# Kernel optimization log

Hardware: AMD Instinct MI355X
Metric: run time of the kernel (lower is better)

The kernel has to match this reference:

```python
import jax, jax.numpy as jnp
import numpy as np

IN_DIM = 512
HEADS = 8
HEAD_DIM = IN_DIM // HEADS
SCALE = HEAD_DIM ** -0.5


def setup_inputs() -> dict:
    key = jax.random.key(0)
    ks = jax.random.split(key, 9)
    B, C, H, W = 16, IN_DIM, 32, 32
    std = 1.0 / np.sqrt(C)  # ~ conv2d default init scale
    inp = {
        "x": jax.random.normal(ks[0], (B, C, H, W), dtype=jnp.float32),
        "wq": jax.random.normal(ks[1], (C, C), dtype=jnp.float32) * std,
        "bq": jax.random.normal(ks[2], (C,), dtype=jnp.float32) * std,
        "wk": jax.random.normal(ks[3], (C, C), dtype=jnp.float32) * std,
        "bk": jax.random.normal(ks[4], (C,), dtype=jnp.float32) * std,
        "wv": jax.random.normal(ks[5], (C, C), dtype=jnp.float32) * std,
        "bv": jax.random.normal(ks[6], (C,), dtype=jnp.float32) * std,
        "wo": jax.random.normal(ks[7], (C, C), dtype=jnp.float32) * std,
        "bo": jax.random.normal(ks[8], (C,), dtype=jnp.float32) * std,
        "gamma": jnp.zeros((1,), dtype=jnp.float32) + 0.1,  # learned residual scale
    }
    return inp


def reference(x, wq, bq, wk, bk, wv, bv, wo, bo, gamma):
    B, C, H, W = x.shape
    N = H * W
    hd = HEAD_DIM
    # flatten spatial: [B, C, N]
    xf = x.reshape(B, C, N)
    # 1x1 convs == channel matmuls: [B, C, N]
    q = jnp.einsum('oc,bcn->bon', wq, xf) + bq[None, :, None]
    k = jnp.einsum('oc,bcn->bon', wk, xf) + bk[None, :, None]
    v = jnp.einsum('oc,bcn->bon', wv, xf) + bv[None, :, None]
    # split heads: [B, heads, head_dim, N]
    q = q.reshape(B, HEADS, hd, N)
    k = k.reshape(B, HEADS, hd, N)
    v = v.reshape(B, HEADS, hd, N)
    # energy[b,h,i,j] = sum_d q[b,h,d,i] * k[b,h,d,j]
    energy = jnp.einsum('bhdi,bhdj->bhij', q, k) * SCALE
    attn = jax.nn.softmax(energy, axis=-1)  # [B, heads, N, N]
    # out[b,h,d,i] = sum_j attn[b,h,i,j] * v[b,h,d,j]
    out = jnp.einsum('bhij,bhdj->bhdi', attn, v)
    out = out.reshape(B, C, N)
    out = jnp.einsum('oc,bcn->bon', wo, out) + bo[None, :, None]
    y = gamma[0] * out.reshape(B, C, H, W) + x
    return y
```

## Files before the change

### kernel.cpp

```cpp
#include <hip/hip_runtime.h>
#include <hip/hip_bf16.h>

#define BB 16
#define CC 512
#define HH 8
#define DD 64
#define NN 1024

using f32x4  = __attribute__((ext_vector_type(4))) float;
typedef __bf16 bf16x8 __attribute__((ext_vector_type(8)));
typedef __bf16 bf16x4 __attribute__((ext_vector_type(4)));

#define MFMA16(a, b, c) __builtin_amdgcn_mfma_f32_16x16x32_bf16((a), (b), (c), 0, 0, 0)

#define WAITVM16 asm volatile("s_waitcnt vmcnt(16)" ::: "memory")
#define WAITVM8  asm volatile("s_waitcnt vmcnt(8)" ::: "memory")
#define WAITVM4  asm volatile("s_waitcnt vmcnt(4)" ::: "memory")
#define WAITVM0  asm volatile("s_waitcnt vmcnt(0)" ::: "memory")
#define BARRIER __builtin_amdgcn_s_barrier()
#define SCHEDB  __builtin_amdgcn_sched_barrier(0)

__device__ __forceinline__ void glds16(const __hip_bfloat16* g, __hip_bfloat16* l) {
  typedef __attribute__((address_space(1))) const void gv_t;
  typedef __attribute__((address_space(3))) void lv_t;
  __builtin_amdgcn_global_load_lds((gv_t*)g, (lv_t*)l, 16, 0, 0);
}

__global__ __launch_bounds__(256) void k_prep(
    const float* __restrict__ x, __hip_bfloat16* __restrict__ xT,
    __hip_bfloat16* __restrict__ xbf,
    const float* __restrict__ wq, const float* __restrict__ wk,
    const float* __restrict__ wv, const float* __restrict__ wo,
    __hip_bfloat16* __restrict__ wqb) {
  __shared__ float tile[64][65];
  const int L = blockIdx.x;
  const int t = threadIdx.x;
  if (L >= 2048) {
    const int j = L - 2048;
    const int mat = j >> 8;
    const float* s = (mat == 0) ? wq : (mat == 1) ? wk : (mat == 2) ? wv : wo;
    __hip_bfloat16* o = wqb + (size_t)mat * CC * CC;
    const int i = ((j & 255) * 256 + t) * 4;
    float4 v = *(const float4*)(s + i);
    alignas(8) __hip_bfloat16 tm[4];
    tm[0] = __float2bfloat16(v.x);
    tm[1] = __float2bfloat16(v.y);
    tm[2] = __float2bfloat16(v.z);
    tm[3] = __float2bfloat16(v.w);
    *(bf16x4*)(o + i) = *(const bf16x4*)tm;
    return;
  }
  const int c = L & 7, r = L >> 3;
  const int b  = c * 2 + (r >> 7);
  const int rr = r & 127;
  const int bn = (rr & 15) * 64;
  const int bc = (rr >> 4) * 64;

  const float* xb = x + ((size_t)b * CC + bc) * NN + bn;
  __hip_bfloat16* xbo = xbf + ((size_t)b * CC + bc) * NN + bn;
  const int r0 = t >> 4;
  const int c0 = (t & 15) * 4;
  for (int p = 0; p < 4; ++p) {
    const int rw = r0 + p * 16;
    float4 v = *(const float4*)(xb + (size_t)rw * NN + c0);
    tile[rw][c0 + 0] = v.x;
    tile[rw][c0 + 1] = v.y;
    tile[rw][c0 + 2] = v.z;
    tile[rw][c0 + 3] = v.w;
    alignas(8) __hip_bfloat16 tm[4];
    tm[0] = __float2bfloat16(v.x);
    tm[1] = __float2bfloat16(v.y);
    tm[2] = __float2bfloat16(v.z);
    tm[3] = __float2bfloat16(v.w);
    *(bf16x4*)(xbo + (size_t)rw * NN + c0) = *(const bf16x4*)tm;
  }
  __syncthreads();

  __hip_bfloat16* xo = xT + ((size_t)b * NN + bn) * CC + bc;
  const int rn0 = t >> 3;
  const int cc0 = (t & 7) * 8;
  for (int p = 0; p < 2; ++p) {
    const int rn = rn0 + p * 32;
    alignas(16) __hip_bfloat16 tmp[8];
    for (int j = 0; j < 8; ++j) tmp[j] = __float2bfloat16(tile[cc0 + j][rn]);
    *(bf16x8*)(xo + (size_t)rn * CC + cc0) = *(const bf16x8*)tmp;
  }
}

__global__ __launch_bounds__(256, 2) void k_gemm_qkv(
    const __hip_bfloat16* __restrict__ Wqkv,
    const __hip_bfloat16* __restrict__ Xt,
    const float* __restrict__ bq, const float* __restrict__ bk,
    const float* __restrict__ bv,
    __hip_bfloat16* __restrict__ qT, __hip_bfloat16* __restrict__ kT,
    __hip_bfloat16* __restrict__ vO, float qscale) {
  __shared__ __hip_bfloat16 Wl[2][8192];
  __shared__ __hip_bfloat16 Xl[2][8192];
  const int bid = blockIdx.x;
  const int by0 = bid >> 7;
  const int bx  = bid & 127;
  const int nt  = bx * 128;
  const int bb  = nt >> 10;
  const int nb  = nt & 1023;
  const int t  = threadIdx.x;
  const int w  = t >> 6, l = t & 63;
  const int wr = w >> 1, wc = w & 1;
  const int lg = l >> 4, lr16 = l & 15;

  f32x4 acc[4][4] = {};

  const int srow = w * 8 + (l >> 3);
  const int scol = ((l & 7) ^ ((l >> 3) & 7)) * 8;
  const __hip_bfloat16* wsrc0 = Wqkv + (size_t)(by0 * 128 + srow) * CC + scol;
  const __hip_bfloat16* xsrc  = Xt + ((size_t)nt + srow) * CC + scol;

  auto STAGE = [&](int bn, int ktg) {
    const int rep = ktg >> 3;
    const int k0  = (ktg & 7) * 64;
    const __hip_bfloat16* ws = wsrc0 + (size_t)rep * 512 * CC;
#pragma unroll
    for (int i = 0; i < 4; ++i)
      glds16(ws + (size_t)(i * 32) * CC + k0, &Wl[bn][(w * 8 + i * 32) * 64]);
#pragma unroll
    for (int i = 0; i < 4; ++i)
      glds16(xsrc + (size_t)(i * 32) * CC + k0, &Xl[bn][(w * 8 + i * 32) * 64]);
  };

  const int s7 = lr16 & 7;
  const int slot0 = ((lg) ^ s7) * 8;
  const int slot1 = ((4 + lg) ^ s7) * 8;
  const int rowA = (wr * 64 + lr16) * 64;
  const int rowB = (wc * 64 + lr16) * 64;

  auto STEP = [&](int bn) {
    const __hip_bfloat16* Wb = &Wl[bn][0];
    const __hip_bfloat16* Xb = &Xl[bn][0];
#pragma unroll
    for (int ks = 0; ks < 2; ++ks) {
      const int sl = ks ? slot1 : slot0;
      bf16x8 af[4], bfr[4];
#pragma unroll
      for (int mi = 0; mi < 4; ++mi) af[mi] = *(const bf16x8*)(Wb + rowA + mi * 1024 + sl);
#pragma unroll
      for (int nj = 0; nj < 4; ++nj) bfr[nj] = *(const bf16x8*)(Xb + rowB + nj * 1024 + sl);
      __builtin_amdgcn_s_setprio(1);
#pragma unroll
      for (int mi = 0; mi < 4; ++mi)
#pragma unroll
        for (int nj = 0; nj < 4; ++nj)
          acc[mi][nj] = MFMA16(af[mi], bfr[nj], acc[mi][nj]);
      __builtin_amdgcn_s_setprio(0);
    }
  };

  STAGE(0, 0);
  STAGE(1, 1);
  for (int ktg = 0; ktg < 24; ++ktg) {
    if (ktg == 23)                    { WAITVM0;  }
    else if (ktg > 0 && (ktg & 7) == 0) { WAITVM16; }
    else                              { WAITVM8;  }
    BARRIER; SCHEDB;
    STEP(ktg & 1);
    BARRIER;
    if (ktg < 22) STAGE(ktg & 1, ktg + 2);

    if ((ktg & 7) == 7) {
      const int rep = ktg >> 3;
      const float* bias = (rep == 0) ? bq : (rep == 1) ? bk : bv;
      const float scale = (rep == 0) ? qscale : 1.0f;
      __hip_bfloat16* outT = (rep == 0) ? qT : kT;
#pragma unroll
      for (int mi = 0; mi < 4; ++mi) {
        const int o0 = by0 * 128 + wr * 64 + mi * 16 + lg * 4;
#pragma unroll
        for (int nj = 0; nj < 4; ++nj) {
          const int n = nb + wc * 64 + nj * 16 + lr16;
          if (rep < 2) {
            alignas(8) __hip_bfloat16 tmp[4];
#pragma unroll
            for (int rj = 0; rj < 4; ++rj)
              tmp[rj] = __float2bfloat16((acc[mi][nj][rj] + bias[o0 + rj]) * scale);
            const int hh = o0 >> 6, d0 = o0 & 63;
            *(bf16x4*)(outT + (((size_t)(bb * HH + hh)) * NN + n) * DD + d0) =
                *(const bf16x4*)tmp;
          } else {
#pragma unroll
            for (int rj = 0; rj < 4; ++rj)
              vO[((size_t)bb * CC + o0 + rj) * NN + n] =
                  __float2bfloat16(acc[mi][nj][rj] + bias[o0 + rj]);
          }
        }
      }
      if (ktg < 23) {
#pragma unroll
        for (int mi = 0; mi < 4; ++mi)
#pragma unroll
          for (int nj = 0; nj < 4; ++nj)
            acc[mi][nj] = f32x4{0.f, 0.f, 0.f, 0.f};
      }
    }
  }
}

__global__ __launch_bounds__(256, 4) void k_gemm_o(
    const __hip_bfloat16* __restrict__ W,
    const __hip_bfloat16* __restrict__ Xt,
    const float* __restrict__ bias,
    const __hip_bfloat16* __restrict__ xbf,
    const float* __restrict__ gamma,
    float* __restrict__ y) {
  __shared__ __hip_bfloat16 Wl[2][4096];
  __shared__ __hip_bfloat16 Xl[2][4096];
  const int b  = blockIdx.z;
  const int ot = blockIdx.y * 128;
  const int nt = blockIdx.x * 128;
  const int t  = threadIdx.x;
  const int w  = t >> 6, l = t & 63;
  const int wr = w >> 1, wc = w & 1;
  const int lg = l >> 4, lr16 = l & 15;

  f32x4 acc[4][4] = {};

  const int srow = w * 16 + (l >> 2);
  const int scol = ((l & 3) ^ ((l >> 3) & 3)) * 8;
  const __hip_bfloat16* ws0 = W + (size_t)(ot + srow) * CC + scol;
  const __hip_bfloat16* xs0 = Xt + ((size_t)b * NN + nt + srow) * CC + scol;

  const int sx  = (lg ^ ((lr16 >> 1) & 3)) * 8;
  const int rdA = (wr * 64 + lr16) * 32 + sx;
  const int rdB = (wc * 64 + lr16) * 32 + sx;

#define STAGEO(bn, k0)                                        \
  do {                                                        \
    glds16(ws0 + (k0), &Wl[bn][w * 512]);                     \
    glds16(ws0 + (size_t)64 * CC + (k0), &Wl[bn][2048 + w * 512]); \
    glds16(xs0 + (k0), &Xl[bn][w * 512]);                     \
    glds16(xs0 + (size_t)64 * CC + (k0), &Xl[bn][2048 + w * 512]); \
  } while (0)

  STAGEO(0, 0);
  for (int kt = 0; kt < 16; ++kt) {
    WAITVM0;
    BARRIER; SCHEDB;
    if (kt < 15) STAGEO((kt + 1) & 1, (kt + 1) * 32);
    const __hip_bfloat16* Wb = &Wl[kt & 1][0];
    const __hip_bfloat16* Xb = &Xl[kt & 1][0];
    bf16x8 af[4], bfr[4];
#pragma unroll
    for (int mi = 0; mi < 4; ++mi) af[mi] = *(const bf16x8*)(Wb + rdA + mi * 512);
#pragma unroll
    for (int nj = 0; nj < 4; ++nj) bfr[nj] = *(const bf16x8*)(Xb + rdB + nj * 512);
    __builtin_amdgcn_s_setprio(1);
#pragma unroll
    for (int mi = 0; mi < 4; ++mi)
#pragma unroll
      for (int nj = 0; nj < 4; ++nj)
        acc[mi][nj] = MFMA16(af[mi], bfr[nj], acc[mi][nj]);
    __builtin_amdgcn_s_setprio(0);
  }
#undef STAGEO

  const float g = gamma[0];
  for (int mi = 0; mi < 4; ++mi) {
    const int o0 = ot + wr * 64 + mi * 16 + lg * 4;
    for (int nj = 0; nj < 4; ++nj) {
      const int n = nt + wc * 64 + nj * 16 + lr16;
      for (int rj = 0; rj < 4; ++rj) {
        const size_t idx = ((size_t)b * CC + o0 + rj) * NN + n;
        y[idx] = g * (acc[mi][nj][rj] + bias[o0 + rj]) + __bfloat162float(xbf[idx]);
      }
    }
  }
}

__global__ __launch_bounds__(256, 2) void k_attn(
    const __hip_bfloat16* __restrict__ qT,
    const __hip_bfloat16* __restrict__ kT,
    const __hip_bfloat16* __restrict__ v,
    __hip_bfloat16* __restrict__ attT) {
  __shared__ __hip_bfloat16 Kl[3][4096];
  __shared__ __hip_bfloat16 Vl[3][4096];

  const int L = blockIdx.x;
  const int c = L & 7, s = L >> 3;
  const int bh = c * 16 + (s >> 2);
  const int i0 = (s & 3) * 256;
  const int b = bh >> 3, h = bh & 7;
  const int t  = threadIdx.x;
  const int w  = t >> 6, l = t & 63;
  const int lg = l >> 4, lr = l & 15;

  const __hip_bfloat16* qb = qT + ((size_t)(b * HH + h)) * NN * DD;
  const __hip_bfloat16* kb = kT + ((size_t)(b * HH + h)) * NN * DD;
  const __hip_bfloat16* vb = v + ((size_t)b * CC + h * DD) * NN;

  bf16x8 qf[4][2];
#pragma unroll
  for (int g = 0; g < 4; ++g) {
    const __hip_bfloat16* qp = qb + (size_t)(i0 + w * 64 + g * 16 + lr) * DD + lg * 8;
    qf[g][0] = *(const bf16x8*)qp;
    qf[g][1] = *(const bf16x8*)(qp + 32);
  }

  const int rA = w * 8 + (l >> 3);
  const int rB = rA + 32;
  const int sA = (l & 7) ^ ((rA & 3) ^ (((rA >> 3) & 1) << 2));
  const __hip_bfloat16* gKA = kb + rA * DD + sA * 8;
  const __hip_bfloat16* gKB = kb + rB * DD + sA * 8;
  const __hip_bfloat16* gVA = vb + (size_t)rA * NN + sA * 8;
  const __hip_bfloat16* gVB = vb + (size_t)rB * NN + sA * 8;

  auto STAGE = [&](int bufn, int tile) {
    glds16(gKA + (size_t)tile * 4096, &Kl[bufn][w * 512]);
    glds16(gKB + (size_t)tile * 4096, &Kl[bufn][2048 + w * 512]);
    glds16(gVA + tile * 64, &Vl[bufn][w * 512]);
    glds16(gVB + tile * 64, &Vl[bufn][2048 + w * 512]);
  };

  const int swzK = (lr & 3) ^ (((lr >> 2) & 1) << 2);
  const int krl  = 8 * (lr >> 2) + (lr & 3);
  const int offK0 = krl * 64 + ((lg ^ swzK) * 8);
  const int offK1 = krl * 64 + (((lg + 4) ^ swzK) * 8);
  const int swzV = (lr & 3) ^ (((lr >> 3) & 1) << 2);

  f32x4 accO[4][4] = {};
  f32x4 accL[4] = {};
  f32x4 st[4][4];
  bf16x8 pf[4][2];
  const bf16x8 ones = {(__bf16)1.f, (__bf16)1.f, (__bf16)1.f, (__bf16)1.f,
                       (__bf16)1.f, (__bf16)1.f, (__bf16)1.f, (__bf16)1.f};

  auto QK = [&](const __hip_bfloat16* Kb) {
    __builtin_amdgcn_s_setprio(1);
#pragma unroll
    for (int jt = 0; jt < 4; ++jt) {
      const int jo = (jt >> 1) * 2048 + (jt & 1) * 256;
      bf16x8 kf0 = *(const bf16x8*)(Kb + jo + offK0);
      bf16x8 kf1 = *(const bf16x8*)(Kb + jo + offK1);
#pragma unroll
      for (int g = 0; g < 4; ++g) {
        f32x4 a = {};
        a = MFMA16(kf0, qf[g][0], a);
        a = MFMA16(kf1, qf[g][1], a);
        st[g][jt] = a;
      }
    }
    __builtin_amdgcn_s_setprio(0);
  };

  auto EXP = [&]() {
#pragma unroll
    for (int g = 0; g < 4; ++g) {
      union { bf16x8 v8; __hip_bfloat16 h[8]; } pk0, pk1;
#pragma unroll
      for (int jt = 0; jt < 4; ++jt)
#pragma unroll
        for (int rj = 0; rj < 4; ++rj) {
          const float p = __builtin_amdgcn_exp2f(st[g][jt][rj]);
          if (jt < 2) pk0.h[(jt & 1) * 4 + rj] = __float2bfloat16(p);
          else        pk1.h[(jt & 1) * 4 + rj] = __float2bfloat16(p);
        }
      pf[g][0] = pk0.v8;
      pf[g][1] = pk1.v8;
    }
  };

  auto PV = [&](const __hip_bfloat16* Vb) {
    __builtin_amdgcn_s_setprio(1);
#pragma unroll
    for (int ks = 0; ks < 2; ++ks) {
#pragma unroll
      for (int dt = 0; dt < 4; ++dt) {
        bf16x8 vf = *(const bf16x8*)(Vb + (dt * 16 + lr) * 64 + (((ks * 4 + lg) ^ swzV) * 8));
#pragma unroll
        for (int g = 0; g < 4; ++g)
          accO[g][dt] = MFMA16(pf[g][ks], vf, accO[g][dt]);
      }
#pragma unroll
      for (int g = 0; g < 4; ++g)
        accL[g] = MFMA16(pf[g][ks], ones, accL[g]);
    }
    __builtin_amdgcn_s_setprio(0);
  };

  STAGE(0, 0);
  STAGE(1, 1);
  STAGE(2, 2);
  WAITVM8;
  BARRIER;
  QK(&Kl[0][0]);
  EXP();

  for (int tl = 0; tl < 16; ++tl) {
    const int cur = tl % 3;
    if (tl < 15) {
      if (tl < 14) { WAITVM4; } else { WAITVM0; }
      BARRIER; SCHEDB;
      QK(&Kl[(tl + 1) % 3][0]);
      PV(&Vl[cur][0]);
      EXP();
      BARRIER;
      if (tl < 13) STAGE(cur, tl + 3);
    } else {
      PV(&Vl[cur][0]);
    }
  }

#pragma unroll
  for (int g = 0; g < 4; ++g)
#pragma unroll
    for (int dt = 0; dt < 4; ++dt) {
      f32x4 o;
#pragma unroll
      for (int rj = 0; rj < 4; ++rj) o[rj] = accO[g][dt][rj] / accL[g][rj];
#pragma unroll
      for (int rj = 0; rj < 4; ++rj) {
        const int i = i0 + w * 64 + g * 16 + 4 * lg + rj;
        const int d = dt * 16 + lr;
        attT[((size_t)b * NN + i) * CC + h * DD + d] = __float2bfloat16(o[rj]);
      }
    }
}

extern "C" void kernel_launch(void* const* d_in, const int* in_sizes, int n_in,
                              void* d_out, int out_size, void* d_ws, size_t ws_size,
                              hipStream_t stream) {
  const float* x     = (const float*)d_in[0];
  const float* wq    = (const float*)d_in[1];
  const float* bq    = (const float*)d_in[2];
  const float* wk    = (const float*)d_in[3];
  const float* bk    = (const float*)d_in[4];
  const float* wv    = (const float*)d_in[5];
  const float* bv    = (const float*)d_in[6];
  const float* wo    = (const float*)d_in[7];
  const float* bo    = (const float*)d_in[8];
  const float* gamma = (const float*)d_in[9];
  float* y = (float*)d_out;

  char* ws = (char*)d_ws;
  const size_t szT = (size_t)BB * NN * CC * 2;
  __hip_bfloat16* xT  = (__hip_bfloat16*)(ws);
  __hip_bfloat16* qT  = (__hip_bfloat16*)(ws + szT);
  __hip_bfloat16* kTb = (__hip_bfloat16*)(ws + 2 * szT);
  __hip_bfloat16* vB  = (__hip_bfloat16*)(ws + 3 * szT);
  __hip_bfloat16* xbf = (__hip_bfloat16*)(ws + 4 * szT);
  __hip_bfloat16* wqb = (__hip_bfloat16*)(ws + 5 * szT);
  __hip_bfloat16* wob = wqb + (size_t)3 * CC * CC;

  k_prep<<<dim3(2048 + 1024), 256, 0, stream>>>(x, xT, xbf, wq, wk, wv, wo, wqb);

  const float qsc = 0.125f * 1.44269504f;
  k_gemm_qkv<<<dim3(512), 256, 0, stream>>>(
      wqb, xT, bq, bk, bv, qT, kTb, vB, qsc);

  k_attn<<<dim3(BB * HH * (NN / 256)), 256, 0, stream>>>(qT, kTb, vB, xT);

  k_gemm_o<<<dim3(NN / 128, CC / 128, BB), 256, 0, stream>>>(
      wob, xT, bo, xbf, gamma, y);
}
```

Measured before the change: 109.7 us.

## Split QKV GEMM into one block per output tile, single-buffered

The QKV projection kernel previously had each of 512 blocks loop over Q, K and V weight sectors using a double-buffered LDS pipeline. Now 1536 blocks each compute one 128x128 output tile over K=512 with a single LDS buffer and a full vmcnt(0) wait every k-step. Occupancy is raised to 4 blocks per CU. This gives more parallelism and less LDS per block, but drops the load/compute overlap within a block and reloads the X tile three times.

New measurement: 111.3 us. Within noise of the previous version (+1.5%).

```diff
diff --git a/kernel.cpp b/kernel.cpp
--- a/kernel.cpp
+++ b/kernel.cpp
@@ -13,7 +13,6 @@
 
 #define MFMA16(a, b, c) __builtin_amdgcn_mfma_f32_16x16x32_bf16((a), (b), (c), 0, 0, 0)
 
-#define WAITVM16 asm volatile("s_waitcnt vmcnt(16)" ::: "memory")
 #define WAITVM8  asm volatile("s_waitcnt vmcnt(8)" ::: "memory")
 #define WAITVM4  asm volatile("s_waitcnt vmcnt(4)" ::: "memory")
 #define WAITVM0  asm volatile("s_waitcnt vmcnt(0)" ::: "memory")
@@ -87,18 +86,19 @@
   }
 }
 
-__global__ __launch_bounds__(256, 2) void k_gemm_qkv(
+__global__ __launch_bounds__(256, 4) void k_gemm_qkv(
     const __hip_bfloat16* __restrict__ Wqkv,
     const __hip_bfloat16* __restrict__ Xt,
     const float* __restrict__ bq, const float* __restrict__ bk,
     const float* __restrict__ bv,
     __hip_bfloat16* __restrict__ qT, __hip_bfloat16* __restrict__ kT,
     __hip_bfloat16* __restrict__ vO, float qscale) {
-  __shared__ __hip_bfloat16 Wl[2][8192];
-  __shared__ __hip_bfloat16 Xl[2][8192];
+  __shared__ __hip_bfloat16 Wl[8192];
+  __shared__ __hip_bfloat16 Xl[8192];
   const int bid = blockIdx.x;
-  const int by0 = bid >> 7;
+  const int by  = bid >> 7;
   const int bx  = bid & 127;
+  const int sector = by >> 2;
   const int nt  = bx * 128;
   const int bb  = nt >> 10;
   const int nb  = nt & 1023;
@@ -111,20 +111,8 @@
 
   const int srow = w * 8 + (l >> 3);
   const int scol = ((l & 7) ^ ((l >> 3) & 7)) * 8;
-  const __hip_bfloat16* wsrc0 = Wqkv + (size_t)(by0 * 128 + srow) * CC + scol;
-  const __hip_bfloat16* xsrc  = Xt + ((size_t)nt + srow) * CC + scol;
-
-  auto STAGE = [&](int bn, int ktg) {
-    const int rep = ktg >> 3;
-    const int k0  = (ktg & 7) * 64;
-    const __hip_bfloat16* ws = wsrc0 + (size_t)rep * 512 * CC;
-#pragma unroll
-    for (int i = 0; i < 4; ++i)
-      glds16(ws + (size_t)(i * 32) * CC + k0, &Wl[bn][(w * 8 + i * 32) * 64]);
-#pragma unroll
-    for (int i = 0; i < 4; ++i)
-      glds16(xsrc + (size_t)(i * 32) * CC + k0, &Xl[bn][(w * 8 + i * 32) * 64]);
-  };
+  const __hip_bfloat16* wsrc = Wqkv + (size_t)(by * 128 + srow) * CC + scol;
+  const __hip_bfloat16* xsrc = Xt + ((size_t)nt + srow) * CC + scol;
 
   const int s7 = lr16 & 7;
   const int slot0 = ((lg) ^ s7) * 8;
@@ -132,17 +120,24 @@
   const int rowA = (wr * 64 + lr16) * 64;
   const int rowB = (wc * 64 + lr16) * 64;
 
-  auto STEP = [&](int bn) {
-    const __hip_bfloat16* Wb = &Wl[bn][0];
-    const __hip_bfloat16* Xb = &Xl[bn][0];
+  for (int kt = 0; kt < 8; ++kt) {
+    const int k0 = kt * 64;
+#pragma unroll
+    for (int i = 0; i < 4; ++i)
+      glds16(wsrc + (size_t)(i * 32) * CC + k0, &Wl[(w * 8 + i * 32) * 64]);
+#pragma unroll
+    for (int i = 0; i < 4; ++i)
+      glds16(xsrc + (size_t)(i * 32) * CC + k0, &Xl[(w * 8 + i * 32) * 64]);
+    WAITVM0;
+    BARRIER; SCHEDB;
 #pragma unroll
     for (int ks = 0; ks < 2; ++ks) {
       const int sl = ks ? slot1 : slot0;
       bf16x8 af[4], bfr[4];
 #pragma unroll
-      for (int mi = 0; mi < 4; ++mi) af[mi] = *(const bf16x8*)(Wb + rowA + mi * 1024 + sl);
-#pragma unroll
-      for (int nj = 0; nj < 4; ++nj) bfr[nj] = *(const bf16x8*)(Xb + rowB + nj * 1024 + sl);
+      for (int mi = 0; mi < 4; ++mi) af[mi] = *(const bf16x8*)(Wl + rowA + mi * 1024 + sl);
+#pragma unroll
+      for (int nj = 0; nj < 4; ++nj) bfr[nj] = *(const bf16x8*)(Xl + rowB + nj * 1024 + sl);
       __builtin_amdgcn_s_setprio(1);
 #pragma unroll
       for (int mi = 0; mi < 4; ++mi)
@@ -151,52 +146,33 @@
           acc[mi][nj] = MFMA16(af[mi], bfr[nj], acc[mi][nj]);
       __builtin_amdgcn_s_setprio(0);
     }
-  };
-
-  STAGE(0, 0);
-  STAGE(1, 1);
-  for (int ktg = 0; ktg < 24; ++ktg) {
-    if (ktg == 23)                    { WAITVM0;  }
-    else if (ktg > 0 && (ktg & 7) == 0) { WAITVM16; }
-    else                              { WAITVM8;  }
-    BARRIER; SCHEDB;
-    STEP(ktg & 1);
     BARRIER;
-    if (ktg < 22) STAGE(ktg & 1, ktg + 2);
-
-    if ((ktg & 7) == 7) {
-      const int rep = ktg >> 3;
-      const float* bias = (rep == 0) ? bq : (rep == 1) ? bk : bv;
-      const float scale = (rep == 0) ? qscale : 1.0f;
-      __hip_bfloat16* outT = (rep == 0) ? qT : kT;
-#pragma unroll
-      for (int mi = 0; mi < 4; ++mi) {
-        const int o0 = by0 * 128 + wr * 64 + mi * 16 + lg * 4;
-#pragma unroll
-        for (int nj = 0; nj < 4; ++nj) {
-          const int n = nb + wc * 64 + nj * 16 + lr16;
-          if (rep < 2) {
-            alignas(8) __hip_bfloat16 tmp[4];
-#pragma unroll
-            for (int rj = 0; rj < 4; ++rj)
-              tmp[rj] = __float2bfloat16((acc[mi][nj][rj] + bias[o0 + rj]) * scale);
-            const int hh = o0 >> 6, d0 = o0 & 63;
-            *(bf16x4*)(outT + (((size_t)(bb * HH + hh)) * NN + n) * DD + d0) =
-                *(const bf16x4*)tmp;
-          } else {
-#pragma unroll
-            for (int rj = 0; rj < 4; ++rj)
-              vO[((size_t)bb * CC + o0 + rj) * NN + n] =
-                  __float2bfloat16(acc[mi][nj][rj] + bias[o0 + rj]);
-          }
-        }
-      }
-      if (ktg < 23) {
-#pragma unroll
-        for (int mi = 0; mi < 4; ++mi)
-#pragma unroll
-          for (int nj = 0; nj < 4; ++nj)
-            acc[mi][nj] = f32x4{0.f, 0.f, 0.f, 0.f};
+  }
+
+  const float* bias = (sector == 0) ? bq : (sector == 1) ? bk : bv;
+  const float scale = (sector == 0) ? qscale : 1.0f;
+  __hip_bfloat16* outT = (sector == 0) ? qT : kT;
+
+#pragma unroll
+  for (int mi = 0; mi < 4; ++mi) {
+    const int og = by * 128 + wr * 64 + mi * 16 + lg * 4;
+    const int o0 = og & 511;
+#pragma unroll
+    for (int nj = 0; nj < 4; ++nj) {
+      const int n = nb + wc * 64 + nj * 16 + lr16;
+      if (sector < 2) {
+        alignas(8) __hip_bfloat16 tmp[4];
+#pragma unroll
+        for (int rj = 0; rj < 4; ++rj)
+          tmp[rj] = __float2bfloat16((acc[mi][nj][rj] + bias[o0 + rj]) * scale);
+        const int hh = o0 >> 6, d0 = o0 & 63;
+        *(bf16x4*)(outT + (((size_t)(bb * HH + hh)) * NN + n) * DD + d0) =
+            *(const bf16x4*)tmp;
+      } else {
+#pragma unroll
+        for (int rj = 0; rj < 4; ++rj)
+          vO[((size_t)bb * CC + o0 + rj) * NN + n] =
+              __float2bfloat16(acc[mi][nj][rj] + bias[o0 + rj]);
       }
     }
   }
@@ -450,7 +426,7 @@
   k_prep<<<dim3(2048 + 1024), 256, 0, stream>>>(x, xT, xbf, wq, wk, wv, wo, wqb);
 
   const float qsc = 0.125f * 1.44269504f;
-  k_gemm_qkv<<<dim3(512), 256, 0, stream>>>(
+  k_gemm_qkv<<<dim3(1536), 256, 0, stream>>>(
       wqb, xT, bq, bk, bv, qT, kTb, vB, qsc);
 
   k_attn<<<dim3(BB * HH * (NN / 256)), 256, 0, stream>>>(qT, kTb, vB, xT);
```
